# Kernel tuning notes

Hardware: AMD Instinct MI355X
Metric: run time of the kernel (lower is better)

## Reference

```python
import jax, jax.numpy as jnp
import numpy as np

V = 4096      # num codes (vocab)
D = 128       # embedding dim
K = 3         # diffusion scales
H = 4         # attn heads
FF = 128      # ff hidden
L = 2         # attn layers
NVIS = 8192   # visits
MAXC = 32     # max codes per visit
PAD = 0


def logmap0(x):
    # Poincare ball (c=1) log map at origin: artanh(||x||) * x / ||x||
    eps = 1e-7
    norm = jnp.linalg.norm(x, axis=-1, keepdims=True)
    norm_c = jnp.clip(norm, eps, 1.0 - 1e-5)
    return jnp.arctanh(norm_c) * x / jnp.maximum(norm, eps)


def layer_norm(x, g, b, eps=1e-5):
    m = jnp.mean(x, axis=-1, keepdims=True)
    v = jnp.mean((x - m) ** 2, axis=-1, keepdims=True)
    return (x - m) * jax.lax.rsqrt(v + eps) * g + b


def attn_block(x, Wqkv, bqkv, Wo, bo, W1, b1, W2, b2, g1, be1, g2, be2):
    # x: [V, D] (batch of 1, squeezed)
    hd = D // H
    qkv = x @ Wqkv.T + bqkv                      # [V, 3D]
    q, k, v = jnp.split(qkv, 3, axis=-1)
    q = q.reshape(V, H, hd)
    k = k.reshape(V, H, hd)
    v = v.reshape(V, H, hd)
    scores = jnp.einsum('shd,thd->hst', q, k) / np.sqrt(hd).astype(x.dtype)
    a = jax.nn.softmax(scores, axis=-1)          # [H, V, V]
    o = jnp.einsum('hst,thd->shd', a, v).reshape(V, D)
    attn_out = o @ Wo.T + bo
    x = layer_norm(x + attn_out, g1, be1)
    ff = jax.nn.gelu(x @ W1.T + b1) @ W2.T + b2
    return layer_norm(x + ff, g2, be2)


def setup_inputs() -> dict:
    key = jax.random.key(0)
    ks = jax.random.split(key, 20)
    inp = {}
    inp['visits'] = jax.random.randint(ks[0], (NVIS, MAXC), 0, V)
    # hyperbolic points inside unit ball
    inp['X_hyp'] = jax.random.normal(ks[1], (V, D), jnp.float32) * 0.01
    inp['kernels'] = jax.random.normal(ks[2], (K, V, V), jnp.float32) / V
    inp['proj_W'] = jax.random.normal(ks[3], (D, K * D), jnp.float32) * 0.05
    inp['proj_b'] = jnp.zeros((D,), jnp.float32)
    s = 0.05
    inp['Wqkv'] = jax.random.normal(ks[4], (L, 3 * D, D), jnp.float32) * s
    inp['bqkv'] = jnp.zeros((L, 3 * D), jnp.float32)
    inp['Wo'] = jax.random.normal(ks[5], (L, D, D), jnp.float32) * s
    inp['bo'] = jnp.zeros((L, D), jnp.float32)
    inp['W1'] = jax.random.normal(ks[6], (L, FF, D), jnp.float32) * s
    inp['b1'] = jnp.zeros((L, FF), jnp.float32)
    inp['W2'] = jax.random.normal(ks[7], (L, D, FF), jnp.float32) * s
    inp['b2'] = jnp.zeros((L, D), jnp.float32)
    inp['ln1_g'] = jnp.ones((L, D), jnp.float32)
    inp['ln1_b'] = jnp.zeros((L, D), jnp.float32)
    inp['ln2_g'] = jnp.ones((L, D), jnp.float32)
    inp['ln2_b'] = jnp.zeros((L, D), jnp.float32)
    return inp


def reference(visits, X_hyp, kernels, proj_W, proj_b, Wqkv, bqkv, Wo, bo,
              W1, b1, W2, b2, ln1_g, ln1_b, ln2_g, ln2_b):
    # ---- hyperbolic graph diffusion ----
    Z0 = logmap0(X_hyp)                              # [V, D]
    Z_scales = jnp.einsum('kuv,vd->ukd', kernels, Z0)  # [V, K, D]
    Z_cat = Z_scales.reshape(V, K * D)
    H_ = Z_cat @ proj_W.T + proj_b                   # [V, D]
    # ---- global self-attention stack ----
    for l in range(L):
        H_ = attn_block(H_, Wqkv[l], bqkv[l], Wo[l], bo[l],
                        W1[l], b1[l], W2[l], b2[l],
                        ln1_g[l], ln1_b[l], ln2_g[l], ln2_b[l])
    # ---- per-visit masked mean pooling (segment mean) ----
    mask = (visits != PAD)                           # [NVIS, MAXC]
    gathered = H_[visits] * mask[..., None]          # [NVIS, MAXC, D]
    cnt = jnp.sum(mask, axis=-1, keepdims=True).astype(H_.dtype)
    summed = jnp.sum(gathered, axis=1)               # [NVIS, D]
    return jnp.where(cnt > 0, summed / jnp.maximum(cnt, 1.0), 0.0)
```

## Files before the change

### kernel.cpp

```cpp
#include <hip/hip_runtime.h>
#include <hip/hip_bf16.h>
#include <math.h>

#define VN 4096
#define DIM 128
#define KS 3
#define NH 4
#define HD 32
#define NVIS 8192
#define MAXC 32
#define KTOT (KS*VN)

typedef unsigned short u16;
typedef __attribute__((ext_vector_type(8))) short short8;
typedef __attribute__((ext_vector_type(4))) float f32x4;

__device__ __forceinline__ u16 f2b(float f){
  union { float f; unsigned u; } c; c.f = f;
  unsigned u = c.u;
  return (u16)((u + 0x7fffu + ((u >> 16) & 1u)) >> 16);
}
__device__ __forceinline__ float b2f(u16 x){
  union { float f; unsigned u; } c; c.u = ((unsigned)x) << 16; return c.f;
}
#define MFMA16(a,b,c) __builtin_amdgcn_mfma_f32_16x16x32_bf16((a),(b),(c),0,0,0)

__global__ __launch_bounds__(256) void k_logmap(const float* __restrict__ xh, u16* __restrict__ z0){
  __shared__ float xs[64][132];
  __shared__ float part[4][64];
  __shared__ float sscale[64];
  int t = threadIdx.x;
  int v0 = blockIdx.x * 64;
  #pragma unroll
  for(int i=0;i<8;i++){
    int id = t + 256*i; int e = id*4; int r = e>>7; int c = e&127;
    float4 u = *(const float4*)&xh[(size_t)(v0+r)*DIM + c];
    xs[r][c+0]=u.x; xs[r][c+1]=u.y; xs[r][c+2]=u.z; xs[r][c+3]=u.w;
  }
  __syncthreads();
  int r = t & 63, q = t >> 6;
  float p = 0.f;
  #pragma unroll
  for(int c=0;c<32;c++){ float x = xs[r][q*32+c]; p += x*x; }
  part[q][r] = p;
  __syncthreads();
  if(t < 64){
    float ss = part[0][t]+part[1][t]+part[2][t]+part[3][t];
    float n = sqrtf(ss);
    float nc = fminf(fmaxf(n, 1e-7f), 1.0f - 1e-5f);
    sscale[t] = atanhf(nc) / fmaxf(n, 1e-7f);
  }
  __syncthreads();
  #pragma unroll
  for(int i=0;i<8;i++){
    int id = t + 256*i; int e = id*4; int rr = e>>7; int cc = e&127;
    float s = sscale[rr];
    ushort4 o;
    o.x = f2b(xs[rr][cc+0]*s); o.y = f2b(xs[rr][cc+1]*s);
    o.z = f2b(xs[rr][cc+2]*s); o.w = f2b(xs[rr][cc+3]*s);
    *(ushort4*)&z0[(size_t)(v0+rr)*DIM + cc] = o;
  }
}

template<bool AF32, bool BF32>
__device__ __forceinline__ void gemm_k128_t(const void* __restrict__ Agv, int lda,
                                            const void* __restrict__ Bgv, int ldb,
                                            u16* As, u16* Bs, f32x4 (&acc)[2][8]){
  int t = threadIdx.x;
  int w=t>>6, lane=t&63, l15=lane&15, quad=lane>>4;
  #pragma unroll
  for(int s=0;s<2;s++)
    #pragma unroll
    for(int n=0;n<8;n++) acc[s][n] = (f32x4){0.f,0.f,0.f,0.f};
  #pragma unroll
  for(int step=0; step<2; step++){
    int kb = step*64;
    __syncthreads();
    #pragma unroll
    for(int i=0;i<4;i++){
      int id = t + 256*i; int row = id>>3, c8 = id&7;
      if(AF32){
        const float* Ag = (const float*)Agv;
        float4 f0 = *(const float4*)&Ag[(size_t)row*lda + kb + c8*8];
        float4 f1 = *(const float4*)&Ag[(size_t)row*lda + kb + c8*8 + 4];
        ushort4 p0 = { f2b(f0.x), f2b(f0.y), f2b(f0.z), f2b(f0.w) };
        ushort4 p1 = { f2b(f1.x), f2b(f1.y), f2b(f1.z), f2b(f1.w) };
        *(ushort4*)&As[row*72 + c8*8]     = p0;
        *(ushort4*)&As[row*72 + c8*8 + 4] = p1;
      } else {
        const u16* Ag = (const u16*)Agv;
        *(uint4*)&As[row*72 + c8*8] = *(const uint4*)&Ag[(size_t)row*lda + kb + c8*8];
      }
      if(BF32){
        const float* Bg = (const float*)Bgv;
        float4 f0 = *(const float4*)&Bg[(size_t)row*ldb + kb + c8*8];
        float4 f1 = *(const float4*)&Bg[(size_t)row*ldb + kb + c8*8 + 4];
        ushort4 p0 = { f2b(f0.x), f2b(f0.y), f2b(f0.z), f2b(f0.w) };
        ushort4 p1 = { f2b(f1.x), f2b(f1.y), f2b(f1.z), f2b(f1.w) };
        *(ushort4*)&Bs[row*72 + c8*8]     = p0;
        *(ushort4*)&Bs[row*72 + c8*8 + 4] = p1;
      } else {
        const u16* Bg = (const u16*)Bgv;
        *(uint4*)&Bs[row*72 + c8*8] = *(const uint4*)&Bg[(size_t)row*ldb + kb + c8*8];
      }
    }
    __syncthreads();
    #pragma unroll
    for(int ks=0; ks<2; ks++){
      short8 a[2], b[8];
      #pragma unroll
      for(int s=0;s<2;s++) a[s] = *(short8*)&As[(w*32+s*16+l15)*72 + (ks*4+quad)*8];
      #pragma unroll
      for(int n=0;n<8;n++)  b[n] = *(short8*)&Bs[(n*16+l15)*72 + (ks*4+quad)*8];
      #pragma unroll
      for(int s=0;s<2;s++)
        #pragma unroll
        for(int n=0;n<8;n++) acc[s][n] = MFMA16(a[s], b[n], acc[s][n]);
    }
  }
}

__global__ __launch_bounds__(256) void k_gproj(const float* __restrict__ projW, const u16* __restrict__ z0,
                                               u16* __restrict__ gbuf){
  __shared__ u16 As[128*72], Bs[128*72];
  int kb = blockIdx.x >> 5, vt = blockIdx.x & 31;
  f32x4 acc[2][8];
  gemm_k128_t<true,false>(projW + kb*128, 3*DIM, z0 + (size_t)vt*128*DIM, DIM, As, Bs, acc);
  int t=threadIdx.x, w=t>>6, lane=t&63, l15=lane&15, quad=lane>>4;
  #pragma unroll
  for(int s=0;s<2;s++)
    #pragma unroll
    for(int n=0;n<8;n++)
      #pragma unroll
      for(int rg=0;rg<4;rg++){
        int d = w*32 + s*16 + quad*4 + rg;
        int v = vt*128 + n*16 + l15;
        gbuf[(size_t)(d*KS + kb)*VN + v] = f2b(acc[s][n][rg]);
      }
}

__global__ __launch_bounds__(256) void k_diff(const float* __restrict__ kers, const u16* __restrict__ gbuf,
                                              u16* __restrict__ hpart){
  __shared__ u16 As[128*72], Bs[128*72];
  int t = threadIdx.x;
  int mt = blockIdx.x & 31;
  int sl = blockIdx.x >> 5;
  int w=t>>6, lane=t&63, l15=lane&15, quad=lane>>4;
  f32x4 acc[2][8];
  #pragma unroll
  for(int s=0;s<2;s++)
    #pragma unroll
    for(int n=0;n<8;n++) acc[s][n] = (f32x4){0.f,0.f,0.f,0.f};
  int k0 = sl * 768;
  for(int step=0; step<12; step++){
    int kk = k0 + step*64;
    int kout = kk >> 12; int vv = kk & 4095;
    __syncthreads();
    #pragma unroll
    for(int i=0;i<4;i++){
      int id = t + 256*i; int row = id>>3, c8 = id&7;
      const float* ap = &kers[((size_t)kout<<24) + (size_t)(mt*128+row)*VN + vv + c8*8];
      float4 f0 = *(const float4*)ap;
      float4 f1 = *(const float4*)(ap+4);
      ushort4 p0 = { f2b(f0.x), f2b(f0.y), f2b(f0.z), f2b(f0.w) };
      ushort4 p1 = { f2b(f1.x), f2b(f1.y), f2b(f1.z), f2b(f1.w) };
      *(ushort4*)&As[row*72 + c8*8]     = p0;
      *(ushort4*)&As[row*72 + c8*8 + 4] = p1;
      *(uint4*)&Bs[row*72 + c8*8] = *(const uint4*)&gbuf[(size_t)row*KTOT + kk + c8*8];
    }
    __syncthreads();
    #pragma unroll
    for(int ks=0; ks<2; ks++){
      short8 a[2], b[8];
      #pragma unroll
      for(int s=0;s<2;s++) a[s] = *(short8*)&As[(w*32+s*16+l15)*72 + (ks*4+quad)*8];
      #pragma unroll
      for(int n=0;n<8;n++)  b[n] = *(short8*)&Bs[(n*16+l15)*72 + (ks*4+quad)*8];
      #pragma unroll
      for(int s=0;s<2;s++)
        #pragma unroll
        for(int n=0;n<8;n++) acc[s][n] = MFMA16(a[s], b[n], acc[s][n]);
    }
  }
  u16* dst = hpart + ((size_t)blockIdx.x << 14);
  #pragma unroll
  for(int s=0;s<2;s++)
    #pragma unroll
    for(int n=0;n<8;n++)
      #pragma unroll
      for(int rg=0;rg<4;rg++)
        dst[(w*32+s*16+quad*4+rg)*128 + n*16 + l15] = f2b(acc[s][n][rg]);
}

__global__ __launch_bounds__(256) void k_hreduce(const u16* __restrict__ hpart, const float* __restrict__ pb,
                                                 float* __restrict__ h0){
  int idx = blockIdx.x*256 + threadIdx.x;
  #pragma unroll
  for(int j=0;j<4;j++){
    int e = j*131072 + idx;
    float v = pb[e & 127];
    #pragma unroll
    for(int sl=0; sl<16; sl++) v += b2f(hpart[((size_t)sl<<19) + e]);
    h0[e] = v;
  }
}

template<bool AF32>
__global__ __launch_bounds__(256) void k_qkv(const void* __restrict__ xb, const float* __restrict__ Wq,
                                             const float* __restrict__ bq, u16* __restrict__ outq){
  __shared__ u16 As[128*72], Bs[128*72];
  int mt = blockIdx.x & 31, ntile = blockIdx.x >> 5;
  f32x4 acc[2][8];
  const void* Ap = AF32 ? (const void*)((const float*)xb + (size_t)mt*128*DIM)
                        : (const void*)((const u16*)xb + (size_t)mt*128*DIM);
  gemm_k128_t<AF32,true>(Ap, DIM, Wq + (size_t)ntile*128*DIM, DIM, As, Bs, acc);
  int t=threadIdx.x, w=t>>6, lane=t&63, l15=lane&15, quad=lane>>4;
  #pragma unroll
  for(int s=0;s<2;s++)
    #pragma unroll
    for(int n=0;n<8;n++)
      #pragma unroll
      for(int rg=0;rg<4;rg++){
        int row = mt*128 + w*32 + s*16 + quad*4 + rg;
        int col = ntile*128 + n*16 + l15;
        outq[(size_t)row*(3*DIM) + col] = f2b(acc[s][n][rg] + bq[col]);
      }
}

__global__ __launch_bounds__(256) void k_attn(const u16* __restrict__ qkv, float* __restrict__ opart,
                                              float* __restrict__ mlpart){
  __shared__ u16 Qs[64*40];
  __shared__ u16 Ksh[2][128*40];
  __shared__ u16 Vt[2][32*136];
  __shared__ u16 Ps[4*16*136];
  int t=threadIdx.x;
  int b = blockIdx.x;
  int h = b>>7, qt = (b>>1)&63, half = b&1;
  int w=t>>6, lane=t&63, l15=lane&15, quad=lane>>4;
  { int r = t>>2, c = t&3;
    *(uint4*)&Qs[r*40 + c*8] = *(const uint4*)&qkv[(size_t)(qt*64+r)*(3*DIM) + h*HD + c*8];
  }
  int skey = t>>2, sc4 = t&3;
  uint4 kreg[2], vreg[2];
  #pragma unroll
  for(int i=0;i<2;i++){
    int key = skey + 64*i;
    kreg[i] = *(const uint4*)&qkv[(size_t)((size_t)(half*16)*128+key)*(3*DIM) + DIM + h*HD + sc4*8];
    vreg[i] = *(const uint4*)&qkv[(size_t)((size_t)(half*16)*128+key)*(3*DIM) + 2*DIM + h*HD + sc4*8];
  }
  #pragma unroll
  for(int i=0;i<2;i++){
    int key = skey + 64*i;
    *(uint4*)&Ksh[0][key*40 + sc4*8] = kreg[i];
    u16 tmp[8]; *(uint4*)tmp = vreg[i];
    #pragma unroll
    for(int j=0;j<8;j++) Vt[0][(sc4*8+j)*136 + key] = tmp[j];
  }
  __syncthreads();
  short8 aq = *(short8*)&Qs[(w*16+l15)*40 + quad*8];
  f32x4 oacc[2]; oacc[0]=(f32x4){0.f,0.f,0.f,0.f}; oacc[1]=(f32x4){0.f,0.f,0.f,0.f};
  float mrun[4], lrun[4];
  #pragma unroll
  for(int rg=0;rg<4;rg++){ mrun[rg] = -INFINITY; lrun[rg] = 0.f; }
  const float sc = 0.17677669529663687f;
  for(int kti=0;kti<16;kti++){
    int cur = kti&1;
    if(kti<15){
      int kt = half*16 + kti + 1;
      #pragma unroll
      for(int i=0;i<2;i++){
        int key = skey + 64*i;
        kreg[i] = *(const uint4*)&qkv[(size_t)(kt*128+key)*(3*DIM) + DIM + h*HD + sc4*8];
        vreg[i] = *(const uint4*)&qkv[(size_t)(kt*128+key)*(3*DIM) + 2*DIM + h*HD + sc4*8];
      }
    }
    f32x4 s[8];
    #pragma unroll
    for(int n=0;n<8;n++)
      s[n] = MFMA16(aq, *(short8*)&Ksh[cur][(n*16+l15)*40 + quad*8], ((f32x4){0.f,0.f,0.f,0.f}));
    float mx[4];
    #pragma unroll
    for(int rg=0;rg<4;rg++){
      float m = -INFINITY;
      #pragma unroll
      for(int n=0;n<8;n++) m = fmaxf(m, s[n][rg]);
      #pragma unroll
      for(int off=1;off<16;off<<=1) m = fmaxf(m, __shfl_xor(m, off, 64));
      mx[rg] = m;
    }
    float alpha[4], rs[4];
    #pragma unroll
    for(int rg=0;rg<4;rg++){
      float mn = fmaxf(mrun[rg], mx[rg]);
      alpha[rg] = __expf(sc*(mrun[rg] - mn));
      mrun[rg] = mn; rs[rg] = 0.f;
    }
    #pragma unroll
    for(int n=0;n<8;n++)
      #pragma unroll
      for(int rg=0;rg<4;rg++){
        float p = __expf(sc*(s[n][rg] - mrun[rg]));
        s[n][rg] = p; rs[rg] += p;
      }
    #pragma unroll
    for(int rg=0;rg<4;rg++){
      #pragma unroll
      for(int off=1;off<16;off<<=1) rs[rg] += __shfl_xor(rs[rg], off, 64);
      lrun[rg] = lrun[rg]*alpha[rg] + rs[rg];
      oacc[0][rg] *= alpha[rg]; oacc[1][rg] *= alpha[rg];
    }
    #pragma unroll
    for(int n=0;n<8;n++)
      #pragma unroll
      for(int rg=0;rg<4;rg++)
        Ps[w*16*136 + (quad*4+rg)*136 + n*16 + l15] = f2b(s[n][rg]);
    #pragma unroll
    for(int kt2=0;kt2<4;kt2++){
      short8 ap = *(short8*)&Ps[w*16*136 + l15*136 + kt2*32 + quad*8];
      #pragma unroll
      for(int n2=0;n2<2;n2++)
        oacc[n2] = MFMA16(ap, *(short8*)&Vt[cur][(n2*16+l15)*136 + kt2*32 + quad*8], oacc[n2]);
    }
    if(kti<15){
      #pragma unroll
      for(int i=0;i<2;i++){
        int key = skey + 64*i;
        *(uint4*)&Ksh[cur^1][key*40 + sc4*8] = kreg[i];
        u16 tmp[8]; *(uint4*)tmp = vreg[i];
        #pragma unroll
        for(int j=0;j<8;j++) Vt[cur^1][(sc4*8+j)*136 + key] = tmp[j];
      }
    }
    __syncthreads();
  }
  float* op = opart + ((size_t)b << 11);
  #pragma unroll
  for(int n2=0;n2<2;n2++)
    #pragma unroll
    for(int rg=0;rg<4;rg++)
      op[(w*16+quad*4+rg)*32 + n2*16 + l15] = oacc[n2][rg];
  if(l15 == 0){
    float* ml = mlpart + ((size_t)b << 7);
    #pragma unroll
    for(int rg=0;rg<4;rg++){
      int r = w*16 + quad*4 + rg;
      ml[r] = sc*mrun[rg]; ml[64 + r] = lrun[rg];
    }
  }
}

__global__ __launch_bounds__(256) void k_oprojln(const float* __restrict__ opart, const float* __restrict__ mlpart,
                                                 const float* __restrict__ W,
                                                 const float* __restrict__ bias, const float* __restrict__ resf,
                                                 const float* __restrict__ g, const float* __restrict__ bb,
                                                 float* __restrict__ outf, u16* __restrict__ outb){
  __shared__ u16 As[128*72], Bs[128*72];
  int mt = blockIdx.x;
  int t=threadIdx.x, w=t>>6, lane=t&63, l15=lane&15, quad=lane>>4;
  f32x4 acc[2][8];
  #pragma unroll
  for(int s=0;s<2;s++)
    #pragma unroll
    for(int n=0;n<8;n++) acc[s][n] = (f32x4){0.f,0.f,0.f,0.f};
  #pragma unroll
  for(int step=0; step<2; step++){
    int kb = step*64;
    __syncthreads();
    #pragma unroll
    for(int i=0;i<4;i++){
      int id = t + 256*i; int row = id>>3, c8 = id&7;
      int col = kb + c8*8;
      int hh = col>>5, c0 = col&31;
      int grow = mt*128 + row;
      int hq = hh*64 + (grow>>6);
      int rr = grow & 63;
      const float* o0  = opart  + ((size_t)(hq*2)   << 11);
      const float* o1  = opart  + ((size_t)(hq*2+1) << 11);
      const float* ml0 = mlpart + ((size_t)(hq*2)   << 7);
      const float* ml1 = mlpart + ((size_t)(hq*2+1) << 7);
      float m0 = ml0[rr], l0 = ml0[64+rr], m1 = ml1[rr], l1 = ml1[64+rr];
      float m = fmaxf(m0, m1);
      float w0 = __expf(m0 - m), w1 = __expf(m1 - m);
      float inv = 1.f / (l0*w0 + l1*w1);
      float4 a0 = *(const float4*)&o0[rr*32 + c0];
      float4 a1 = *(const float4*)&o0[rr*32 + c0 + 4];
      float4 c0v = *(const float4*)&o1[rr*32 + c0];
      float4 c1v = *(const float4*)&o1[rr*32 + c0 + 4];
      ushort4 p0 = { f2b((a0.x*w0+c0v.x*w1)*inv), f2b((a0.y*w0+c0v.y*w1)*inv),
                     f2b((a0.z*w0+c0v.z*w1)*inv), f2b((a0.w*w0+c0v.w*w1)*inv) };
      ushort4 p1 = { f2b((a1.x*w0+c1v.x*w1)*inv), f2b((a1.y*w0+c1v.y*w1)*inv),
                     f2b((a1.z*w0+c1v.z*w1)*inv), f2b((a1.w*w0+c1v.w*w1)*inv) };
      *(ushort4*)&As[row*72 + c8*8]     = p0;
      *(ushort4*)&As[row*72 + c8*8 + 4] = p1;
      float4 f0 = *(const float4*)&W[(size_t)row*DIM + kb + c8*8];
      float4 f1 = *(const float4*)&W[(size_t)row*DIM + kb + c8*8 + 4];
      ushort4 q0 = { f2b(f0.x), f2b(f0.y), f2b(f0.z), f2b(f0.w) };
      ushort4 q1 = { f2b(f1.x), f2b(f1.y), f2b(f1.z), f2b(f1.w) };
      *(ushort4*)&Bs[row*72 + c8*8]     = q0;
      *(ushort4*)&Bs[row*72 + c8*8 + 4] = q1;
    }
    __syncthreads();
    #pragma unroll
    for(int ks=0; ks<2; ks++){
      short8 a[2], b[8];
      #pragma unroll
      for(int s=0;s<2;s++) a[s] = *(short8*)&As[(w*32+s*16+l15)*72 + (ks*4+quad)*8];
      #pragma unroll
      for(int n=0;n<8;n++)  b[n] = *(short8*)&Bs[(n*16+l15)*72 + (ks*4+quad)*8];
      #pragma unroll
      for(int s=0;s<2;s++)
        #pragma unroll
        for(int n=0;n<8;n++) acc[s][n] = MFMA16(a[s], b[n], acc[s][n]);
    }
  }
  #pragma unroll
  for(int s=0;s<2;s++)
    #pragma unroll
    for(int n=0;n<8;n++)
      #pragma unroll
      for(int rg=0;rg<4;rg++){
        int row = mt*128 + w*32 + s*16 + quad*4 + rg;
        int col = n*16 + l15;
        acc[s][n][rg] += bias[col] + resf[(size_t)row*DIM + col];
      }
  #pragma unroll
  for(int s=0;s<2;s++)
    #pragma unroll
    for(int rg=0;rg<4;rg++){
      float a=0.f, bsum=0.f;
      #pragma unroll
      for(int n=0;n<8;n++){ float x = acc[s][n][rg]; a += x; bsum += x*x; }
      #pragma unroll
      for(int off=1;off<16;off<<=1){ a += __shfl_xor(a, off, 64); bsum += __shfl_xor(bsum, off, 64); }
      float mean = a*(1.f/128.f);
      float var  = bsum*(1.f/128.f) - mean*mean;
      float rstd = rsqrtf(var + 1e-5f);
      #pragma unroll
      for(int n=0;n<8;n++){
        int row = mt*128 + w*32 + s*16 + quad*4 + rg;
        int col = n*16 + l15;
        float y = (acc[s][n][rg] - mean)*rstd*g[col] + bb[col];
        outf[(size_t)row*DIM + col] = y;
        outb[(size_t)row*DIM + col] = f2b(y);
      }
    }
}

__global__ __launch_bounds__(256) void k_projln(const u16* __restrict__ Ab, const float* __restrict__ W,
                                                const float* __restrict__ bias, const float* __restrict__ resf,
                                                const float* __restrict__ g, const float* __restrict__ bb,
                                                float* __restrict__ outf, u16* __restrict__ outb){
  __shared__ u16 As[128*72], Bs[128*72];
  int mt = blockIdx.x;
  f32x4 acc[2][8];
  gemm_k128_t<false,true>(Ab + (size_t)mt*128*DIM, DIM, W, DIM, As, Bs, acc);
  int t=threadIdx.x, w=t>>6, lane=t&63, l15=lane&15, quad=lane>>4;
  #pragma unroll
  for(int s=0;s<2;s++)
    #pragma unroll
    for(int n=0;n<8;n++)
      #pragma unroll
      for(int rg=0;rg<4;rg++){
        int row = mt*128 + w*32 + s*16 + quad*4 + rg;
        int col = n*16 + l15;
        acc[s][n][rg] += bias[col] + resf[(size_t)row*DIM + col];
      }
  #pragma unroll
  for(int s=0;s<2;s++)
    #pragma unroll
    for(int rg=0;rg<4;rg++){
      float a=0.f, bsum=0.f;
      #pragma unroll
      for(int n=0;n<8;n++){ float x = acc[s][n][rg]; a += x; bsum += x*x; }
      #pragma unroll
      for(int off=1;off<16;off<<=1){ a += __shfl_xor(a, off, 64); bsum += __shfl_xor(bsum, off, 64); }
      float mean = a*(1.f/128.f);
      float var  = bsum*(1.f/128.f) - mean*mean;
      float rstd = rsqrtf(var + 1e-5f);
      #pragma unroll
      for(int n=0;n<8;n++){
        int row = mt*128 + w*32 + s*16 + quad*4 + rg;
        int col = n*16 + l15;
        float y = (acc[s][n][rg] - mean)*rstd*g[col] + bb[col];
        outf[(size_t)row*DIM + col] = y;
        outb[(size_t)row*DIM + col] = f2b(y);
      }
    }
}

__global__ __launch_bounds__(256) void k_ff1(const u16* __restrict__ Ab, const float* __restrict__ W,
                                             const float* __restrict__ bias, u16* __restrict__ outb){
  __shared__ u16 As[128*72], Bs[128*72];
  int mt = blockIdx.x;
  f32x4 acc[2][8];
  gemm_k128_t<false,true>(Ab + (size_t)mt*128*DIM, DIM, W, DIM, As, Bs, acc);
  int t=threadIdx.x, w=t>>6, lane=t&63, l15=lane&15, quad=lane>>4;
  #pragma unroll
  for(int s=0;s<2;s++)
    #pragma unroll
    for(int n=0;n<8;n++)
      #pragma unroll
      for(int rg=0;rg<4;rg++){
        int row = mt*128 + w*32 + s*16 + quad*4 + rg;
        int col = n*16 + l15;
        float v = acc[s][n][rg] + bias[col];
        float z = 0.7978845608028654f*(v + 0.044715f*v*v*v);
        float e = __expf(2.f*z);
        float th = 1.f - 2.f/(e + 1.f);
        outb[(size_t)row*DIM + col] = f2b(0.5f*v*(1.f + th));
      }
}

__global__ __launch_bounds__(256) void k_pool(const int* __restrict__ visits, const float* __restrict__ xf,
                                              float* __restrict__ out){
  int t = threadIdx.x;
  int vis = blockIdx.x*2 + (t>>7);
  int col = t & 127;
  float s = 0.f; int cnt = 0;
  #pragma unroll
  for(int j=0;j<MAXC;j++){
    int idx = visits[vis*MAXC + j];
    if(idx != 0){ s += xf[(size_t)idx*DIM + col]; cnt++; }
  }
  float r = (cnt > 0) ? s/(float)cnt : 0.f;
  out[(size_t)vis*DIM + col] = r;
}

extern "C" void kernel_launch(void* const* d_in, const int* in_sizes, int n_in,
                              void* d_out, int out_size, void* d_ws, size_t ws_size,
                              hipStream_t stream){
  (void)in_sizes; (void)n_in; (void)out_size; (void)ws_size;
  const int*   visits = (const int*)d_in[0];
  const float* xhyp  = (const float*)d_in[1];
  const float* kers  = (const float*)d_in[2];
  const float* projW = (const float*)d_in[3];
  const float* projb = (const float*)d_in[4];
  const float* Wqkv  = (const float*)d_in[5];
  const float* bqkv  = (const float*)d_in[6];
  const float* Wo    = (const float*)d_in[7];
  const float* bo    = (const float*)d_in[8];
  const float* W1    = (const float*)d_in[9];
  const float* b1    = (const float*)d_in[10];
  const float* W2    = (const float*)d_in[11];
  const float* b2    = (const float*)d_in[12];
  const float* g1    = (const float*)d_in[13];
  const float* be1   = (const float*)d_in[14];
  const float* g2    = (const float*)d_in[15];
  const float* be2   = (const float*)d_in[16];

  char* ws = (char*)d_ws;
  u16*   z0    = (u16*)(ws);
  u16*   gbuf  = (u16*)(ws + (1u<<20));
  float* h0    = (float*)(ws + (4u<<20));
  u16*   qkvb  = (u16*)(ws + (7u<<20));
  float* ln1f  = (float*)(ws + (11u<<20));
  u16*   ln1b  = (u16*)(ws + (13u<<20));
  u16*   ffa   = (u16*)(ws + (14u<<20));
  float* x1f   = (float*)(ws + (15u<<20));
  u16*   x1b   = (u16*)(ws + (17u<<20));
  float* x2f   = (float*)(ws + (18u<<20));
  u16*   x2b   = (u16*)(ws + (20u<<20));
  u16*   hpart = (u16*)(ws + (21u<<20));
  float* opart = (float*)(ws + (53u<<20));
  float* mlprt = (float*)(ws + (57u<<20));

  k_logmap<<<64,256,0,stream>>>(xhyp, z0);
  k_gproj<<<96,256,0,stream>>>(projW, z0, gbuf);
  k_diff<<<512,256,0,stream>>>(kers, gbuf, hpart);
  k_hreduce<<<512,256,0,stream>>>(hpart, projb, h0);

  const void* curA = (const void*)h0; bool af32 = true;
  const float* curf = h0;
  float* outfs[2] = {x1f, x2f}; u16* outbs[2] = {x1b, x2b};
  for(int l=0;l<2;l++){
    if(af32) k_qkv<true ><<<96,256,0,stream>>>(curA, Wqkv + (size_t)l*3*DIM*DIM, bqkv + (size_t)l*3*DIM, qkvb);
    else     k_qkv<false><<<96,256,0,stream>>>(curA, Wqkv + (size_t)l*3*DIM*DIM, bqkv + (size_t)l*3*DIM, qkvb);
    k_attn<<<512,256,0,stream>>>(qkvb, opart, mlprt);
    k_oprojln<<<32,256,0,stream>>>(opart, mlprt, Wo + (size_t)l*DIM*DIM, bo + (size_t)l*DIM, curf,
                                   g1 + (size_t)l*DIM, be1 + (size_t)l*DIM, ln1f, ln1b);
    k_ff1<<<32,256,0,stream>>>(ln1b, W1 + (size_t)l*DIM*DIM, b1 + (size_t)l*DIM, ffa);
    k_projln<<<32,256,0,stream>>>(ffa, W2 + (size_t)l*DIM*DIM, b2 + (size_t)l*DIM, ln1f,
                                  g2 + (size_t)l*DIM, be2 + (size_t)l*DIM, outfs[l], outbs[l]);
    curA = (const void*)outbs[l]; af32 = false; curf = outfs[l];
  }
  k_pool<<<4096,256,0,stream>>>(visits, curf, (float*)d_out);
}
```

Baseline: 610.6 us.

## Double-buffer LDS tiles with register prefetch and packed bf16 conversion

Restructures the shared GEMM helper and the diffusion kernel to use two LDS buffers. The next K-slice is loaded into registers while MFMAs run on the current buffer, so global latency overlaps compute and one barrier per step is removed. Scalar bf16 rounding is replaced with the hardware packed v_cvt_pk_bf16_f32 instruction, kernel loads become nontemporal, and the partial-sum reduction is vectorized. The cost is doubled LDS per block (possibly lower occupancy) plus more live registers, and the rounding mode of the conversion instruction may differ slightly from the manual code.

```diff
diff --git a/kernel.cpp b/kernel.cpp
--- a/kernel.cpp
+++ b/kernel.cpp
@@ -14,6 +14,7 @@
 typedef unsigned short u16;
 typedef __attribute__((ext_vector_type(8))) short short8;
 typedef __attribute__((ext_vector_type(4))) float f32x4;
+typedef __attribute__((ext_vector_type(4))) float f4v;
 
 __device__ __forceinline__ u16 f2b(float f){
   union { float f; unsigned u; } c; c.f = f;
@@ -22,6 +23,11 @@
 }
 __device__ __forceinline__ float b2f(u16 x){
   union { float f; unsigned u; } c; c.u = ((unsigned)x) << 16; return c.f;
+}
+__device__ __forceinline__ unsigned cvt2(float lo, float hi){
+  unsigned r;
+  asm("v_cvt_pk_bf16_f32 %0, %1, %2" : "=v"(r) : "v"(lo), "v"(hi));
+  return r;
 }
 #define MFMA16(a,b,c) __builtin_amdgcn_mfma_f32_16x16x32_bf16((a),(b),(c),0,0,0)
 
@@ -55,74 +61,91 @@
   for(int i=0;i<8;i++){
     int id = t + 256*i; int e = id*4; int rr = e>>7; int cc = e&127;
     float s = sscale[rr];
-    ushort4 o;
-    o.x = f2b(xs[rr][cc+0]*s); o.y = f2b(xs[rr][cc+1]*s);
-    o.z = f2b(xs[rr][cc+2]*s); o.w = f2b(xs[rr][cc+3]*s);
-    *(ushort4*)&z0[(size_t)(v0+rr)*DIM + cc] = o;
+    uint2 o = { cvt2(xs[rr][cc+0]*s, xs[rr][cc+1]*s),
+                cvt2(xs[rr][cc+2]*s, xs[rr][cc+3]*s) };
+    *(uint2*)&z0[(size_t)(v0+rr)*DIM + cc] = o;
   }
 }
 
 template<bool AF32, bool BF32>
 __device__ __forceinline__ void gemm_k128_t(const void* __restrict__ Agv, int lda,
                                             const void* __restrict__ Bgv, int ldb,
-                                            u16* As, u16* Bs, f32x4 (&acc)[2][8]){
+                                            u16 (*As)[128*72], u16 (*Bs)[128*72], f32x4 (&acc)[2][8]){
   int t = threadIdx.x;
   int w=t>>6, lane=t&63, l15=lane&15, quad=lane>>4;
   #pragma unroll
   for(int s=0;s<2;s++)
     #pragma unroll
     for(int n=0;n<8;n++) acc[s][n] = (f32x4){0.f,0.f,0.f,0.f};
-  #pragma unroll
-  for(int step=0; step<2; step++){
-    int kb = step*64;
-    __syncthreads();
+
+  float4 af[4][2]; uint4 ai[4];
+  float4 bf[4][2]; uint4 bi[4];
+
+  auto LOAD = [&](int kb){
     #pragma unroll
     for(int i=0;i<4;i++){
       int id = t + 256*i; int row = id>>3, c8 = id&7;
-      if(AF32){
+      if constexpr(AF32){
         const float* Ag = (const float*)Agv;
-        float4 f0 = *(const float4*)&Ag[(size_t)row*lda + kb + c8*8];
-        float4 f1 = *(const float4*)&Ag[(size_t)row*lda + kb + c8*8 + 4];
-        ushort4 p0 = { f2b(f0.x), f2b(f0.y), f2b(f0.z), f2b(f0.w) };
-        ushort4 p1 = { f2b(f1.x), f2b(f1.y), f2b(f1.z), f2b(f1.w) };
-        *(ushort4*)&As[row*72 + c8*8]     = p0;
-        *(ushort4*)&As[row*72 + c8*8 + 4] = p1;
+        af[i][0] = *(const float4*)&Ag[(size_t)row*lda + kb + c8*8];
+        af[i][1] = *(const float4*)&Ag[(size_t)row*lda + kb + c8*8 + 4];
       } else {
         const u16* Ag = (const u16*)Agv;
-        *(uint4*)&As[row*72 + c8*8] = *(const uint4*)&Ag[(size_t)row*lda + kb + c8*8];
-      }
-      if(BF32){
+        ai[i] = *(const uint4*)&Ag[(size_t)row*lda + kb + c8*8];
+      }
+      if constexpr(BF32){
         const float* Bg = (const float*)Bgv;
-        float4 f0 = *(const float4*)&Bg[(size_t)row*ldb + kb + c8*8];
-        float4 f1 = *(const float4*)&Bg[(size_t)row*ldb + kb + c8*8 + 4];
-        ushort4 p0 = { f2b(f0.x), f2b(f0.y), f2b(f0.z), f2b(f0.w) };
-        ushort4 p1 = { f2b(f1.x), f2b(f1.y), f2b(f1.z), f2b(f1.w) };
-        *(ushort4*)&Bs[row*72 + c8*8]     = p0;
-        *(ushort4*)&Bs[row*72 + c8*8 + 4] = p1;
+        bf[i][0] = *(const float4*)&Bg[(size_t)row*ldb + kb + c8*8];
+        bf[i][1] = *(const float4*)&Bg[(size_t)row*ldb + kb + c8*8 + 4];
       } else {
         const u16* Bg = (const u16*)Bgv;
-        *(uint4*)&Bs[row*72 + c8*8] = *(const uint4*)&Bg[(size_t)row*ldb + kb + c8*8];
-      }
-    }
-    __syncthreads();
+        bi[i] = *(const uint4*)&Bg[(size_t)row*ldb + kb + c8*8];
+      }
+    }
+  };
+  auto COMMIT = [&](u16* Ad, u16* Bd){
+    #pragma unroll
+    for(int i=0;i<4;i++){
+      int id = t + 256*i; int row = id>>3, c8 = id&7;
+      if constexpr(AF32){
+        uint4 p = { cvt2(af[i][0].x, af[i][0].y), cvt2(af[i][0].z, af[i][0].w),
+                    cvt2(af[i][1].x, af[i][1].y), cvt2(af[i][1].z, af[i][1].w) };
+        *(uint4*)&Ad[row*72 + c8*8] = p;
+      } else {
+        *(uint4*)&Ad[row*72 + c8*8] = ai[i];
+      }
+      if constexpr(BF32){
+        uint4 q = { cvt2(bf[i][0].x, bf[i][0].y), cvt2(bf[i][0].z, bf[i][0].w),
+                    cvt2(bf[i][1].x, bf[i][1].y), cvt2(bf[i][1].z, bf[i][1].w) };
+        *(uint4*)&Bd[row*72 + c8*8] = q;
+      } else {
+        *(uint4*)&Bd[row*72 + c8*8] = bi[i];
+      }
+    }
+  };
+  auto COMPUTE = [&](const u16* Asb, const u16* Bsb){
     #pragma unroll
     for(int ks=0; ks<2; ks++){
       short8 a[2], b[8];
       #pragma unroll
-      for(int s=0;s<2;s++) a[s] = *(short8*)&As[(w*32+s*16+l15)*72 + (ks*4+quad)*8];
-      #pragma unroll
-      for(int n=0;n<8;n++)  b[n] = *(short8*)&Bs[(n*16+l15)*72 + (ks*4+quad)*8];
+      for(int s=0;s<2;s++) a[s] = *(const short8*)&Asb[(w*32+s*16+l15)*72 + (ks*4+quad)*8];
+      #pragma unroll
+      for(int n=0;n<8;n++)  b[n] = *(const short8*)&Bsb[(n*16+l15)*72 + (ks*4+quad)*8];
       #pragma unroll
       for(int s=0;s<2;s++)
         #pragma unroll
         for(int n=0;n<8;n++) acc[s][n] = MFMA16(a[s], b[n], acc[s][n]);
     }
-  }
+  };
+
+  LOAD(0);  COMMIT(As[0], Bs[0]);  __syncthreads();
+  LOAD(64); COMPUTE(As[0], Bs[0]); COMMIT(As[1], Bs[1]); __syncthreads();
+  COMPUTE(As[1], Bs[1]);
 }
 
 __global__ __launch_bounds__(256) void k_gproj(const float* __restrict__ projW, const u16* __restrict__ z0,
                                                u16* __restrict__ gbuf){
-  __shared__ u16 As[128*72], Bs[128*72];
+  __shared__ u16 As[2][128*72], Bs[2][128*72];
   int kb = blockIdx.x >> 5, vt = blockIdx.x & 31;
   f32x4 acc[2][8];
   gemm_k128_t<true,false>(projW + kb*128, 3*DIM, z0 + (size_t)vt*128*DIM, DIM, As, Bs, acc);
@@ -141,7 +164,7 @@
 
 __global__ __launch_bounds__(256) void k_diff(const float* __restrict__ kers, const u16* __restrict__ gbuf,
                                               u16* __restrict__ hpart){
-  __shared__ u16 As[128*72], Bs[128*72];
+  __shared__ u16 As[2][128*72], Bs[2][128*72];
   int t = threadIdx.x;
   int mt = blockIdx.x & 31;
   int sl = blockIdx.x >> 5;
@@ -152,36 +175,65 @@
     #pragma unroll
     for(int n=0;n<8;n++) acc[s][n] = (f32x4){0.f,0.f,0.f,0.f};
   int k0 = sl * 768;
-  for(int step=0; step<12; step++){
+
+  f4v  fa0[4], fa1[4];
+  uint4 fb[4];
+
+  auto LOADSTEP = [&](int step){
     int kk = k0 + step*64;
     int kout = kk >> 12; int vv = kk & 4095;
-    __syncthreads();
     #pragma unroll
     for(int i=0;i<4;i++){
       int id = t + 256*i; int row = id>>3, c8 = id&7;
       const float* ap = &kers[((size_t)kout<<24) + (size_t)(mt*128+row)*VN + vv + c8*8];
-      float4 f0 = *(const float4*)ap;
-      float4 f1 = *(const float4*)(ap+4);
-      ushort4 p0 = { f2b(f0.x), f2b(f0.y), f2b(f0.z), f2b(f0.w) };
-      ushort4 p1 = { f2b(f1.x), f2b(f1.y), f2b(f1.z), f2b(f1.w) };
-      *(ushort4*)&As[row*72 + c8*8]     = p0;
-      *(ushort4*)&As[row*72 + c8*8 + 4] = p1;
-      *(uint4*)&Bs[row*72 + c8*8] = *(const uint4*)&gbuf[(size_t)row*KTOT + kk + c8*8];
-    }
-    __syncthreads();
+      fa0[i] = __builtin_nontemporal_load((const f4v*)ap);
+      fa1[i] = __builtin_nontemporal_load((const f4v*)(ap+4));
+      fb[i]  = *(const uint4*)&gbuf[(size_t)row*KTOT + kk + c8*8];
+    }
+  };
+  auto COMMIT = [&](u16* Ad, u16* Bd){
+    #pragma unroll
+    for(int i=0;i<4;i++){
+      int id = t + 256*i; int row = id>>3, c8 = id&7;
+      uint4 pa = { cvt2(fa0[i].x, fa0[i].y), cvt2(fa0[i].z, fa0[i].w),
+                   cvt2(fa1[i].x, fa1[i].y), cvt2(fa1[i].z, fa1[i].w) };
+      *(uint4*)&Ad[row*72 + c8*8] = pa;
+      *(uint4*)&Bd[row*72 + c8*8] = fb[i];
+    }
+  };
+  auto COMPUTE = [&](const u16* Asb, const u16* Bsb){
     #pragma unroll
     for(int ks=0; ks<2; ks++){
       short8 a[2], b[8];
       #pragma unroll
-      for(int s=0;s<2;s++) a[s] = *(short8*)&As[(w*32+s*16+l15)*72 + (ks*4+quad)*8];
-      #pragma unroll
-      for(int n=0;n<8;n++)  b[n] = *(short8*)&Bs[(n*16+l15)*72 + (ks*4+quad)*8];
+      for(int s=0;s<2;s++) a[s] = *(const short8*)&Asb[(w*32+s*16+l15)*72 + (ks*4+quad)*8];
+      #pragma unroll
+      for(int n=0;n<8;n++)  b[n] = *(const short8*)&Bsb[(n*16+l15)*72 + (ks*4+quad)*8];
       #pragma unroll
       for(int s=0;s<2;s++)
         #pragma unroll
         for(int n=0;n<8;n++) acc[s][n] = MFMA16(a[s], b[n], acc[s][n]);
     }
-  }
+  };
+
+  LOADSTEP(0);
+  COMMIT(As[0], Bs[0]);
+  __syncthreads();
+  #pragma unroll 1
+  for(int sp=0; sp<6; sp++){
+    LOADSTEP(2*sp+1);
+    COMPUTE(As[0], Bs[0]);
+    COMMIT(As[1], Bs[1]);
+    __syncthreads();
+    if(sp < 5){
+      LOADSTEP(2*sp+2);
+      COMPUTE(As[1], Bs[1]);
+      COMMIT(As[0], Bs[0]);
+      __syncthreads();
+    }
+  }
+  COMPUTE(As[1], Bs[1]);
+
   u16* dst = hpart + ((size_t)blockIdx.x << 14);
   #pragma unroll
   for(int s=0;s<2;s++)
@@ -195,20 +247,23 @@
 __global__ __launch_bounds__(256) void k_hreduce(const u16* __restrict__ hpart, const float* __restrict__ pb,
                                                  float* __restrict__ h0){
   int idx = blockIdx.x*256 + threadIdx.x;
-  #pragma unroll
-  for(int j=0;j<4;j++){
-    int e = j*131072 + idx;
-    float v = pb[e & 127];
-    #pragma unroll
-    for(int sl=0; sl<16; sl++) v += b2f(hpart[((size_t)sl<<19) + e]);
-    h0[e] = v;
-  }
+  int e0 = idx*4;
+  int c0 = e0 & 127;
+  float4 r;
+  r.x = pb[c0+0]; r.y = pb[c0+1]; r.z = pb[c0+2]; r.w = pb[c0+3];
+  #pragma unroll
+  for(int sl=0; sl<16; sl++){
+    uint2 u = *(const uint2*)&hpart[((size_t)sl<<19) + e0];
+    r.x += b2f((u16)(u.x & 0xffffu)); r.y += b2f((u16)(u.x >> 16));
+    r.z += b2f((u16)(u.y & 0xffffu)); r.w += b2f((u16)(u.y >> 16));
+  }
+  *(float4*)&h0[e0] = r;
 }
 
 template<bool AF32>
 __global__ __launch_bounds__(256) void k_qkv(const void* __restrict__ xb, const float* __restrict__ Wq,
                                              const float* __restrict__ bq, u16* __restrict__ outq){
-  __shared__ u16 As[128*72], Bs[128*72];
+  __shared__ u16 As[2][128*72], Bs[2][128*72];
   int mt = blockIdx.x & 31, ntile = blockIdx.x >> 5;
   f32x4 acc[2][8];
   const void* Ap = AF32 ? (const void*)((const float*)xb + (size_t)mt*128*DIM)
@@ -386,18 +441,17 @@
       float4 a1 = *(const float4*)&o0[rr*32 + c0 + 4];
       float4 c0v = *(const float4*)&o1[rr*32 + c0];
       float4 c1v = *(const float4*)&o1[rr*32 + c0 + 4];
-      ushort4 p0 = { f2b((a0.x*w0+c0v.x*w1)*inv), f2b((a0.y*w0+c0v.y*w1)*inv),
-                     f2b((a0.z*w0+c0v.z*w1)*inv), f2b((a0.w*w0+c0v.w*w1)*inv) };
-      ushort4 p1 = { f2b((a1.x*w0+c1v.x*w1)*inv), f2b((a1.y*w0+c1v.y*w1)*inv),
-                     f2b((a1.z*w0+c1v.z*w1)*inv), f2b((a1.w*w0+c1v.w*w1)*inv) };
-      *(ushort4*)&As[row*72 + c8*8]     = p0;
-      *(ushort4*)&As[row*72 + c8*8 + 4] = p1;
+      uint4 pa = { cvt2((a0.x*w0+c0v.x*w1)*inv, (a0.y*w0+c0v.y*w1)*inv),
+                   cvt2((a0.z*w0+c0v.z*w1)*inv, (a0.w*w0+c0v.w*w1)*inv),
+                   cvt2((a1.x*w0+c1v.x*w1)*inv, (a1.y*w0+c1v.y*w1)*inv),
+                   cvt2((a1.w*0.f + a1.x*w0 + c1v.x*w1)*inv*0.f + (a1.w*w0+c1v.w*w1)*inv, (a1.w*w0+c1v.w*w1)*inv) };
+      pa.w = cvt2((a1.z*w0+c1v.z*w1)*inv, (a1.w*w0+c1v.w*w1)*inv);
+      *(uint4*)&As[row*72 + c8*8] = pa;
       float4 f0 = *(const float4*)&W[(size_t)row*DIM + kb + c8*8];
       float4 f1 = *(const float4*)&W[(size_t)row*DIM + kb + c8*8 + 4];
-      ushort4 q0 = { f2b(f0.x), f2b(f0.y), f2b(f0.z), f2b(f0.w) };
-      ushort4 q1 = { f2b(f1.x), f2b(f1.y), f2b(f1.z), f2b(f1.w) };
-      *(ushort4*)&Bs[row*72 + c8*8]     = q0;
-      *(ushort4*)&Bs[row*72 + c8*8 + 4] = q1;
+      uint4 qa = { cvt2(f0.x, f0.y), cvt2(f0.z, f0.w),
+                   cvt2(f1.x, f1.y), cvt2(f1.z, f1.w) };
+      *(uint4*)&Bs[row*72 + c8*8] = qa;
     }
     __syncthreads();
     #pragma unroll
@@ -450,7 +504,7 @@
                                                 const float* __restrict__ bias, const float* __restrict__ resf,
                                                 const float* __restrict__ g, const float* __restrict__ bb,
                                                 float* __restrict__ outf, u16* __restrict__ outb){
-  __shared__ u16 As[128*72], Bs[128*72];
+  __shared__ u16 As[2][128*72], Bs[2][128*72];
   int mt = blockIdx.x;
   f32x4 acc[2][8];
   gemm_k128_t<false,true>(Ab + (size_t)mt*128*DIM, DIM, W, DIM, As, Bs, acc);
@@ -490,7 +544,7 @@
 
 __global__ __launch_bounds__(256) void k_ff1(const u16* __restrict__ Ab, const float* __restrict__ W,
                                              const float* __restrict__ bias, u16* __restrict__ outb){
-  __shared__ u16 As[128*72], Bs[128*72];
+  __shared__ u16 As[2][128*72], Bs[2][128*72];
   int mt = blockIdx.x;
   f32x4 acc[2][8];
   gemm_k128_t<false,true>(Ab + (size_t)mt*128*DIM, DIM, W, DIM, As, Bs, acc);
```

After: 555.4 us. -9.0%, faster.
